# Performance work log

Measured on AMD Instinct MI355X. Metric: run time of the kernel, lower is better.

## Reference

```python
import jax, jax.numpy as jnp
import numpy as np

B, K, N, D, H, DD, NB, SEQ = 1, 512, 16384, 512, 64, 64, 10, 2048
COREF_PROP = 1  # config['coref_prop']
BIG = 1e23      # additive mask penalty from the torch code


def bucket_distance(d):
    # Lee et al. style log buckets: 0,1,2,3,4, [5-7], [8-15], [16-31], [32-63], [64+]
    d = jnp.abs(d)
    logb = jnp.floor(jnp.log2(jnp.maximum(d, 1).astype(jnp.float32))).astype(d.dtype) + 3
    return jnp.clip(jnp.where(d < 5, d, logb), 0, NB - 1)


def setup_inputs() -> dict:
    key = jax.random.key(0)
    ks = jax.random.split(key, 20)
    rng = np.random.default_rng(0)
    s = 0.02
    span_begin = jnp.sort(jax.random.randint(ks[2], (B, K), 0, SEQ), axis=-1)
    return dict(
        all_span_vecs=jax.random.normal(ks[0], (B, N, D), jnp.float32),
        span_vecs=jax.random.normal(ks[1], (B, K, D), jnp.float32),
        span_begin=span_begin,
        span_end=span_begin + jax.random.randint(ks[3], (B, K), 1, 10),
        triangular_mask=jnp.broadcast_to(jnp.tril(jnp.ones((K, K), jnp.float32), -1), (B, K, K)),
        span_scores=jax.random.normal(ks[4], (B, K, 1), jnp.float32),
        prune_indices=jnp.asarray(np.sort(np.stack([rng.choice(N, K, replace=False) for _ in range(B)]), axis=-1), jnp.int32),
        span_lengths=jnp.full((B,), K, jnp.int32),
        sequence_lengths=jnp.full((B,), SEQ, jnp.int32),
        Wl=jax.random.normal(ks[5], (D, H)) * s, bl=jnp.zeros((H,), jnp.float32),
        Wr=jax.random.normal(ks[6], (D, H)) * s, br=jnp.zeros((H,), jnp.float32),
        Wp=jax.random.normal(ks[7], (D, H)) * s,
        dist_emb=jax.random.normal(ks[8], (NB, DD)) * s,
        Wd=jax.random.normal(ks[9], (DD, H)) * s, bd=jnp.zeros((H,), jnp.float32),
        Wo=jax.random.normal(ks[10], (H, 1)) * s, bo=jnp.zeros((1,), jnp.float32),
        Wg1=jax.random.normal(ks[11], (2 * D, D)) * s, bg1=jnp.zeros((D,), jnp.float32),
        Wg2=jax.random.normal(ks[12], (2 * D, D)) * s, bg2=jnp.zeros((D,), jnp.float32),
        Wpr=jax.random.normal(ks[13], (D, 1)) * s, bpr=jnp.zeros((1,), jnp.float32),
    )


def reference(all_span_vecs, span_vecs, span_begin, span_end, triangular_mask,
              span_scores, prune_indices, span_lengths, sequence_lengths,
              Wl, bl, Wr, br, Wp, dist_emb, Wd, bd, Wo, bo,
              Wg1, bg1, Wg2, bg2, Wpr, bpr):
    # ----- OptFFpairs pairwise scorer: relu(left_i + right_j + prod(v_i*v_j) + dist_ij) -> scalar
    dist_idx = bucket_distance(span_begin[:, :, None] - span_begin[:, None, :])  # [B,K,K]
    dist_feat = dist_emb[dist_idx] @ Wd + bd                                     # [B,K,K,H]

    def pair_scores(u):
        left = u @ Wl + bl                                  # [B,K,H]
        right = u @ Wr + br                                 # [B,K,H]
        prod = jnp.einsum('bid,bjd,dh->bijh', u, u, Wp)     # avoids [B,K,K,D] intermediate
        h = jax.nn.relu(left[:, :, None, :] + right[:, None, :, :] + prod + dist_feat)
        return (h @ Wo + bo)[..., 0]                        # [B,K,K], i.e. squeeze(-1)

    eye = jnp.eye(K, dtype=span_vecs.dtype)[None]

    def add_scores(cs, ss):  # coref_add_scores: add span scores as rows+cols, zero diagonal
        cs = cs + ss + jnp.swapaxes(ss, -1, -2)
        return cs * (1.0 - eye)

    def gate(Wg, bg, left, right):  # MyGate: g = sigmoid(W[l;r]); g*l + (1-g)*r
        g = jax.nn.sigmoid(jnp.concatenate([left, right], -1) @ Wg + bg)
        return g * left + (1.0 - g) * right

    update = span_vecs
    cs = add_scores(pair_scores(update), span_scores)
    m1 = (1.0 - triangular_mask) * BIG
    m2 = (1.0 - jnp.swapaxes(triangular_mask, 1, 2)) * BIG
    for _ in range(COREF_PROP):
        p1 = jax.nn.softmax(cs - m1, axis=-1)
        p2 = jax.nn.softmax(cs - m2, axis=-1)
        c1 = p1 @ update
        c2 = p2 @ update
        update = gate(Wg1, bg1, update, c1) + gate(Wg2, bg2, update, c2)
        # update_coref_scores=True: rescore with pruner(update)
        cs = add_scores(pair_scores(update), update @ Wpr + bpr)

    # ----- overwrite_spans: masked scatter of updated filtered spans into all spans
    mask = (jnp.arange(K)[None, :] < span_lengths[:, None])[..., None]  # [B,K,1]
    b_idx = jnp.arange(B)[:, None]
    orig = all_span_vecs[b_idx, prune_indices]                          # [B,K,D]
    all_out = all_span_vecs.at[b_idx, prune_indices].set(jnp.where(mask, update, orig))
    return all_out, update, cs
```

## Files before the change

### kernel.cpp

```cpp
#include <hip/hip_runtime.h>
#include <hip/hip_bf16.h>


typedef __bf16 bf16;
typedef bf16 bf16x8 __attribute__((ext_vector_type(8)));
typedef float f32x4 __attribute__((ext_vector_type(4)));
typedef float f32x16 __attribute__((ext_vector_type(16)));

#define MFMA16(a, b, c) __builtin_amdgcn_mfma_f32_16x16x32_bf16((a), (b), (c), 0, 0, 0)
#define MFMA32(a, b, c) __builtin_amdgcn_mfma_f32_32x32x16_bf16((a), (b), (c), 0, 0, 0)

__device__ __forceinline__ void gll16(const bf16* g, bf16* lds) {
  __builtin_amdgcn_global_load_lds(
      (const __attribute__((address_space(1))) unsigned int*)g,
      (__attribute__((address_space(3))) unsigned int*)lds, 16, 0, 0);
}

__global__ void k_prep(const float* __restrict__ sv,
                       const float* __restrict__ Wl, const float* __restrict__ Wr,
                       const float* __restrict__ Wg1, const float* __restrict__ Wg2,
                       const float* __restrict__ de, const float* __restrict__ Wd,
                       const float* __restrict__ bd, const float* __restrict__ bl,
                       const float* __restrict__ br, const float* __restrict__ bg1,
                       const float* __restrict__ bg2, const float* __restrict__ Wp,
                       bf16* __restrict__ u1, bf16* __restrict__ ugb,
                       bf16* __restrict__ wlr, float* __restrict__ blbr,
                       float* __restrict__ bgc, bf16* __restrict__ wgb,
                       float* __restrict__ dtab, bf16* __restrict__ wpTb)
{
  const int total = 262144 + 65536 + 128 + 1048576 + 1024 + 640 + 32768;
  for (int idx0 = blockIdx.x * 256 + threadIdx.x; idx0 < total; idx0 += 2048 * 256) {
    int k = idx0;
    if (k < 262144) {
      float v = sv[k]; bf16 b = (bf16)v; u1[k] = b;
      int i = k >> 9, d = k & 511;
      ugb[(long)i * 1024 + d] = b;
      ugb[524288 + (long)i * 1024 + d] = b;
      continue;
    }
    k -= 262144;
    if (k < 65536) {
      int d = k >> 7, h = k & 127;
      wlr[k] = (bf16)(h < 64 ? Wl[d * 64 + h] : Wr[d * 64 + h - 64]);
      continue;
    }
    k -= 65536;
    if (k < 128) { blbr[k] = (k < 64 ? bl[k] : br[k - 64]); continue; }
    k -= 128;
    if (k < 1048576) {
      wgb[k] = (bf16)(k < 524288 ? Wg1[k] : Wg2[k - 524288]);
      continue;
    }
    k -= 1048576;
    if (k < 1024) { bgc[k] = (k < 512 ? bg1[k] : bg2[k - 512]); continue; }
    k -= 1024;
    if (k < 640) {
      int b_ = k >> 6, h = k & 63;
      float s = bd[h];
      for (int e = 0; e < 64; ++e) s += de[b_ * 64 + e] * Wd[e * 64 + h];
      dtab[k] = s;
      continue;
    }
    k -= 640;
    {
      int h = k >> 9, d = k & 511;
      wpTb[k] = (bf16)Wp[d * 64 + h];
    }
  }
}

__global__ __launch_bounds__(256, 2) void k_gemm(
    const bf16* __restrict__ A, int lda, long asz,
    const bf16* __restrict__ B, int ldb, long bsz,
    float* __restrict__ C, int ldc, long csz,
    const float* __restrict__ bias, int bstride, int K,
    bf16* __restrict__ xout)
{
  __shared__ bf16 As[64 * 40];
  __shared__ bf16 Bs[64 * 40];
  const int t = threadIdx.x, lane = t & 63, wave = t >> 6;
  const int tc = blockIdx.x, tr = blockIdx.y, z = blockIdx.z;
  A += (long)z * asz; B += (long)z * bsz; C += (long)z * csz;
  const int wr = wave >> 1, wc = wave & 1;
  const int arow = t >> 2, aslot = t & 3;
  const int s = lane >> 4, rr = lane & 15;
  f32x4 acc00 = {}, acc01 = {}, acc10 = {}, acc11 = {};
  const int nk = K >> 5;
  for (int kk = 0; kk < nk; ++kk) {
    __syncthreads();
    *(uint4*)&As[arow * 40 + aslot * 8] =
        *(const uint4*)(A + (long)(tr * 64 + arow) * lda + kk * 32 + aslot * 8);
    {
      const bf16* bsrc = B + (long)(kk * 32 + aslot * 8) * ldb + tc * 64 + arow;
      bf16x8 tv;
#pragma unroll
      for (int e = 0; e < 8; ++e) tv[e] = bsrc[(long)e * ldb];
      *(bf16x8*)&Bs[arow * 40 + aslot * 8] = tv;
    }
    __syncthreads();
    bf16x8 a0 = *(const bf16x8*)&As[(wr * 32 + rr) * 40 + s * 8];
    bf16x8 a1 = *(const bf16x8*)&As[(wr * 32 + 16 + rr) * 40 + s * 8];
    bf16x8 b0 = *(const bf16x8*)&Bs[(wc * 32 + rr) * 40 + s * 8];
    bf16x8 b1 = *(const bf16x8*)&Bs[(wc * 32 + 16 + rr) * 40 + s * 8];
    acc00 = MFMA16(a0, b0, acc00);
    acc01 = MFMA16(a0, b1, acc01);
    acc10 = MFMA16(a1, b0, acc10);
    acc11 = MFMA16(a1, b1, acc11);
  }
#pragma unroll
  for (int mf = 0; mf < 2; ++mf) {
#pragma unroll
    for (int nf = 0; nf < 2; ++nf) {
      f32x4 v = mf == 0 ? (nf == 0 ? acc00 : acc01) : (nf == 0 ? acc10 : acc11);
      int col = tc * 64 + wc * 32 + nf * 16 + rr;
      float bi = bias ? bias[z * bstride + col] : 0.f;
      int row0 = tr * 64 + wr * 32 + mf * 16 + s * 4;
#pragma unroll
      for (int r = 0; r < 4; ++r) {
        float val = v[r] + bi;
        int row = row0 + r;
        C[(long)row * ldc + col] = val;
        if (xout) {
          long gidx = (row < 512)
              ? ((long)row * 1024 + 512 + col)
              : (524288 + (long)(row - 512) * 1024 + 512 + col);
          xout[gidx] = (bf16)val;
        }
      }
    }
  }
}

__global__ __launch_bounds__(512, 2) void k_pair(
    const bf16* __restrict__ Ubf, const float* __restrict__ Uf,
    const bf16* __restrict__ wpTb, const float* __restrict__ LR,
    const float* __restrict__ dtabg, const int* __restrict__ sb,
    const float* __restrict__ ss, const float* __restrict__ Wo,
    const float* __restrict__ bo, float* __restrict__ cs,
    const float* __restrict__ copysrc, float* __restrict__ copydst, int docopy)
{
  __shared__ bf16 Apan[2][256 * 32];
  __shared__ bf16 Bpan[2][256 * 32];
  __shared__ float dtsp[10 * 68];
  __shared__ int sbt[256];

  const int t = threadIdx.x;
  const int l = t & 63;
  const int w = t >> 6;
  const int wm = w >> 1, wn = w & 1;
  const int hi = l >> 5, l31 = l & 31;
  const int jb = blockIdx.x;
  const int mt = blockIdx.y;
  const int i0 = mt * 4;
  const int i = i0 + wm;

  for (int idx = t; idx < 640; idx += 512)
    dtsp[(idx >> 6) * 68 + (idx & 63)] = dtabg[idx];
  if (t < 256) sbt[t] = sb[jb * 256 + t];

  const bf16 *bsrc0, *bsrc1;
  {
    int r0 = t >> 2, c0 = t & 3;
    int r1 = 128 + (t >> 2);
    bsrc0 = Ubf + (long)(jb * 256 + r0) * 512 + ((c0 ^ ((r0 >> 1) & 3)) * 8);
    bsrc1 = Ubf + (long)(jb * 256 + r1) * 512 + ((c0 ^ ((r1 >> 1) & 3)) * 8);
  }
  const int ar0 = t >> 2, ar1 = 128 + (t >> 2), as0 = t & 3;
  const int awb0 = ar0 * 64 + ((as0 ^ ((ar0 >> 1) & 3)) * 16);
  const int awb1 = ar1 * 64 + ((as0 ^ ((ar1 >> 1) & 3)) * 16);
  const float* ua0p = Uf + (long)(i0 + (ar0 >> 6)) * 512 + as0 * 8;
  const float* ua1p = Uf + (long)(i0 + (ar1 >> 6)) * 512 + as0 * 8;
  const bf16* wp0p = wpTb + (long)(ar0 & 63) * 512 + as0 * 8;
  const bf16* wp1p = wpTb + (long)(ar1 & 63) * 512 + as0 * 8;

  int aoff[2][2], boff[4][2];
#pragma unroll
  for (int rf = 0; rf < 2; ++rf)
#pragma unroll
    for (int ks = 0; ks < 2; ++ks) {
      int r = wm * 64 + rf * 32 + l31;
      aoff[rf][ks] = r * 64 + (((ks * 2 + hi) ^ ((r >> 1) & 3)) * 16);
    }
#pragma unroll
  for (int cf = 0; cf < 4; ++cf)
#pragma unroll
    for (int ks = 0; ks < 2; ++ks) {
      int r = wn * 128 + cf * 32 + l31;
      boff[cf][ks] = r * 64 + (((ks * 2 + hi) ^ ((r >> 1) & 3)) * 16);
    }

  {
    gll16(bsrc0, &Bpan[0][0 * 4096 + w * 512]);
    gll16(bsrc1, &Bpan[0][1 * 4096 + w * 512]);
    float4 a00 = *(const float4*)ua0p, a01 = *(const float4*)(ua0p + 4);
    float4 a10 = *(const float4*)ua1p, a11 = *(const float4*)(ua1p + 4);
    bf16x8 w0 = *(const bf16x8*)wp0p, w1 = *(const bf16x8*)wp1p;
    bf16x8 v0, v1;
#pragma unroll
    for (int e = 0; e < 4; ++e) {
      v0[e] = (bf16)(a00[e] * (float)w0[e]);
      v0[e + 4] = (bf16)(a01[e] * (float)w0[e + 4]);
      v1[e] = (bf16)(a10[e] * (float)w1[e]);
      v1[e + 4] = (bf16)(a11[e] * (float)w1[e + 4]);
    }
    *(bf16x8*)((char*)&Apan[0][0] + awb0) = v0;
    *(bf16x8*)((char*)&Apan[0][0] + awb1) = v1;
  }
  asm volatile("s_waitcnt vmcnt(0)");
  __syncthreads();

  f32x16 acc[2][4] = {};

  for (int kc = 0; kc < 16; ++kc) {
    const int cur = kc & 1;
    float4 nA00, nA01, nA10, nA11;
    bf16x8 nW0, nW1;
    if (kc < 15) {
      gll16(bsrc0 + (kc + 1) * 32, &Bpan[cur ^ 1][0 * 4096 + w * 512]);
      gll16(bsrc1 + (kc + 1) * 32, &Bpan[cur ^ 1][1 * 4096 + w * 512]);
      nA00 = *(const float4*)(ua0p + (kc + 1) * 32);
      nA01 = *(const float4*)(ua0p + (kc + 1) * 32 + 4);
      nA10 = *(const float4*)(ua1p + (kc + 1) * 32);
      nA11 = *(const float4*)(ua1p + (kc + 1) * 32 + 4);
      nW0 = *(const bf16x8*)(wp0p + (kc + 1) * 32);
      nW1 = *(const bf16x8*)(wp1p + (kc + 1) * 32);
    }
    const char* Ab = (const char*)&Apan[cur][0];
    const char* Bb = (const char*)&Bpan[cur][0];
#pragma unroll
    for (int ks = 0; ks < 2; ++ks) {
      bf16x8 af0 = *(const bf16x8*)(Ab + aoff[0][ks]);
      bf16x8 af1 = *(const bf16x8*)(Ab + aoff[1][ks]);
      bf16x8 bf0 = *(const bf16x8*)(Bb + boff[0][ks]);
      bf16x8 bf1 = *(const bf16x8*)(Bb + boff[1][ks]);
      bf16x8 bf2 = *(const bf16x8*)(Bb + boff[2][ks]);
      bf16x8 bf3 = *(const bf16x8*)(Bb + boff[3][ks]);
      __builtin_amdgcn_s_setprio(1);
      acc[0][0] = MFMA32(af0, bf0, acc[0][0]);
      acc[0][1] = MFMA32(af0, bf1, acc[0][1]);
      acc[0][2] = MFMA32(af0, bf2, acc[0][2]);
      acc[0][3] = MFMA32(af0, bf3, acc[0][3]);
      acc[1][0] = MFMA32(af1, bf0, acc[1][0]);
      acc[1][1] = MFMA32(af1, bf1, acc[1][1]);
      acc[1][2] = MFMA32(af1, bf2, acc[1][2]);
      acc[1][3] = MFMA32(af1, bf3, acc[1][3]);
      __builtin_amdgcn_s_setprio(0);
    }
    if (kc < 15) {
      asm volatile("s_waitcnt vmcnt(0)");
      bf16x8 v0, v1;
#pragma unroll
      for (int e = 0; e < 4; ++e) {
        v0[e] = (bf16)(nA00[e] * (float)nW0[e]);
        v0[e + 4] = (bf16)(nA01[e] * (float)nW0[e + 4]);
        v1[e] = (bf16)(nA10[e] * (float)nW1[e]);
        v1[e + 4] = (bf16)(nA11[e] * (float)nW1[e + 4]);
      }
      *(bf16x8*)((char*)&Apan[cur ^ 1][0] + awb0) = v0;
      *(bf16x8*)((char*)&Apan[cur ^ 1][0] + awb1) = v1;
    }
    __syncthreads();
  }

  float4 wo_t[2][4], lf_t[2][4];
#pragma unroll
  for (int rf = 0; rf < 2; ++rf)
#pragma unroll
    for (int g = 0; g < 4; ++g) {
      wo_t[rf][g] = *(const float4*)&Wo[rf * 32 + 4 * hi + 8 * g];
      lf_t[rf][g] = *(const float4*)&LR[i * 128 + rf * 32 + 4 * hi + 8 * g];
    }
  const float ssi = ss[i];
  const int sbi = sb[i];
  const float bo0 = bo[0];
#pragma unroll
  for (int cf = 0; cf < 4; ++cf) {
    int jl = wn * 128 + cf * 32 + l31;
    int j = jb * 256 + jl;
    int dd = sbi - sbt[jl];
    int ad = dd < 0 ? -dd : dd;
    int bkt = ad < 5 ? ad : (31 - __clz(ad)) + 3;
    bkt = bkt > 9 ? 9 : bkt;
    float ssj = ss[j];
    float sum = 0.f;
#pragma unroll
    for (int rf = 0; rf < 2; ++rf) {
#pragma unroll
      for (int g = 0; g < 4; ++g) {
        float4 dt4 = *(const float4*)&dtsp[bkt * 68 + rf * 32 + 4 * hi + 8 * g];
        float4 rt4 = *(const float4*)&LR[j * 128 + 64 + rf * 32 + 4 * hi + 8 * g];
#pragma unroll
        for (int e = 0; e < 4; ++e) {
          float v = acc[rf][cf][g * 4 + e] + lf_t[rf][g][e] + rt4[e] + dt4[e];
          v = fmaxf(v, 0.f);
          sum += v * wo_t[rf][g][e];
        }
      }
    }
    sum += __shfl_xor(sum, 32);
    float val = (j == i) ? 0.f : (sum + bo0 + ssi + ssj);
    if (hi == 0) cs[(long)i * 512 + j] = val;
  }

  if (docopy) {
    const float4* s4 = (const float4*)copysrc;
    float4* d4 = (float4*)copydst;
    int idx = (mt * 2 + jb) * 512 + t;
#pragma unroll
    for (int q = 0; q < 16; ++q)
      d4[(long)q * 131072 + idx] = s4[(long)q * 131072 + idx];
  }
}

__global__ __launch_bounds__(64) void k_softmax(const float* __restrict__ cs,
                                                bf16* __restrict__ p12)
{
  int b = blockIdx.x, kind = b >> 9, i = b & 511, lane = threadIdx.x;
  const float* row = cs + i * 512;
  float v[8];
  float4 x0 = *(const float4*)(row + lane * 8);
  float4 x1 = *(const float4*)(row + lane * 8 + 4);
  v[0] = x0.x; v[1] = x0.y; v[2] = x0.z; v[3] = x0.w;
  v[4] = x1.x; v[5] = x1.y; v[6] = x1.z; v[7] = x1.w;
  bool any = (kind == 0) ? (i > 0) : (i < 511);
  bf16x8 ov;
  if (!any) {
    float u = 1.0f / 512.0f;
#pragma unroll
    for (int e = 0; e < 8; ++e) ov[e] = (bf16)u;
  } else {
    float m = -3.4e38f;
#pragma unroll
    for (int e = 0; e < 8; ++e) {
      int jj = lane * 8 + e;
      bool valid = (kind == 0) ? (jj < i) : (jj > i);
      if (valid) m = fmaxf(m, v[e]);
    }
    m = fmaxf(m, __shfl_xor(m, 1));  m = fmaxf(m, __shfl_xor(m, 2));
    m = fmaxf(m, __shfl_xor(m, 4));  m = fmaxf(m, __shfl_xor(m, 8));
    m = fmaxf(m, __shfl_xor(m, 16)); m = fmaxf(m, __shfl_xor(m, 32));
    float p[8]; float ssum = 0.f;
#pragma unroll
    for (int e = 0; e < 8; ++e) {
      int jj = lane * 8 + e;
      bool valid = (kind == 0) ? (jj < i) : (jj > i);
      p[e] = valid ? __expf(v[e] - m) : 0.f;
      ssum += p[e];
    }
    ssum += __shfl_xor(ssum, 1);  ssum += __shfl_xor(ssum, 2);
    ssum += __shfl_xor(ssum, 4);  ssum += __shfl_xor(ssum, 8);
    ssum += __shfl_xor(ssum, 16); ssum += __shfl_xor(ssum, 32);
    float inv = 1.0f / ssum;
#pragma unroll
    for (int e = 0; e < 8; ++e) ov[e] = (bf16)(p[e] * inv);
  }
  *(bf16x8*)(p12 + (long)b * 512 + lane * 8) = ov;
}

__global__ __launch_bounds__(512) void k_mid2(
    const float* __restrict__ sv, const float* __restrict__ c12,
    const float* __restrict__ G12, const float* __restrict__ Wpr,
    const float* __restrict__ bpr, const bf16* __restrict__ wlr,
    const float* __restrict__ blbr, const int* __restrict__ pi,
    const int* __restrict__ sl, float* __restrict__ upd,
    bf16* __restrict__ u2, float* __restrict__ ss2,
    float* __restrict__ lr2, float* __restrict__ out_all)
{
  __shared__ float upl[512];
  __shared__ float red[8];
  __shared__ float part2[4][128];
  const int i = blockIdx.x;
  const int t = threadIdx.x;
  const long ii = (long)i * 512 + t;

  float u = sv[ii], c1 = c12[ii], c2 = c12[262144 + ii];
  float g1 = 1.f / (1.f + __expf(-G12[ii]));
  float g2 = 1.f / (1.f + __expf(-G12[262144 + ii]));
  float up = g1 * u + (1.f - g1) * c1 + g2 * u + (1.f - g2) * c2;
  upd[ii] = up;
  u2[ii] = (bf16)up;
  upl[t] = up;
  if (i < sl[0]) out_all[(long)pi[i] * 512 + t] = up;

  float pd = up * Wpr[t];
  pd += __shfl_xor(pd, 1);  pd += __shfl_xor(pd, 2);  pd += __shfl_xor(pd, 4);
  pd += __shfl_xor(pd, 8);  pd += __shfl_xor(pd, 16); pd += __shfl_xor(pd, 32);
  if ((t & 63) == 0) red[t >> 6] = pd;
  __syncthreads();
  if (t == 0) {
    float s = 0.f;
#pragma unroll
    for (int e = 0; e < 8; ++e) s += red[e];
    ss2[i] = s + bpr[0];
  }

  const int n = t & 127, part = t >> 7;
  float s = 0.f;
  const int d0 = part * 128;
#pragma unroll 4
  for (int d2 = 0; d2 < 128; ++d2)
    s += upl[d0 + d2] * (float)wlr[(d0 + d2) * 128 + n];
  part2[part][n] = s;
  __syncthreads();
  if (t < 128)
    lr2[(long)i * 128 + t] =
        part2[0][t] + part2[1][t] + part2[2][t] + part2[3][t] + blbr[t];
}

extern "C" void kernel_launch(void* const* d_in, const int* in_sizes, int n_in,
                              void* d_out, int out_size, void* d_ws, size_t ws_size,
                              hipStream_t stream)
{
  const float* asv = (const float*)d_in[0];
  const float* sv = (const float*)d_in[1];
  const int* sb = (const int*)d_in[2];
  const float* sscore = (const float*)d_in[5];
  const int* pi = (const int*)d_in[6];
  const int* sl = (const int*)d_in[7];
  const float* Wl = (const float*)d_in[9];
  const float* bl = (const float*)d_in[10];
  const float* Wr = (const float*)d_in[11];
  const float* br = (const float*)d_in[12];
  const float* Wp = (const float*)d_in[13];
  const float* de = (const float*)d_in[14];
  const float* Wd = (const float*)d_in[15];
  const float* bd = (const float*)d_in[16];
  const float* Wo = (const float*)d_in[17];
  const float* bo = (const float*)d_in[18];
  const float* Wg1 = (const float*)d_in[19];
  const float* bg1 = (const float*)d_in[20];
  const float* Wg2 = (const float*)d_in[21];
  const float* bg2 = (const float*)d_in[22];
  const float* Wpr = (const float*)d_in[23];
  const float* bpr = (const float*)d_in[24];

  float* out_all = (float*)d_out;
  float* out_upd = out_all + 8388608;
  float* out_cs = out_all + 8650752;

  char* w = (char*)d_ws;
  size_t off = 0;
  auto take = [&](size_t bytes) -> void* {
    void* p = w + off;
    off = (off + bytes + 255) & ~(size_t)255;
    return p;
  };
  bf16* u1b = (bf16*)take(524288);
  bf16* u2b = (bf16*)take(524288);
  bf16* wlr = (bf16*)take(131072);
  bf16* wgb = (bf16*)take(2097152);
  float* blbr = (float*)take(512);
  float* bgc = (float*)take(4096);
  float* dtab = (float*)take(2560);
  bf16* wpTb = (bf16*)take(65536);
  float* lr1 = (float*)take(262144);
  float* lr2 = (float*)take(262144);
  float* cs1 = (float*)take(1048576);
  bf16* p12 = (bf16*)take(1048576);
  float* c12 = (float*)take(4194304);
  bf16* ugb = (bf16*)take(2097152);
  float* G12 = (float*)take(2097152);
  float* ss2 = (float*)take(2048);

  k_prep<<<2048, 256, 0, stream>>>(sv, Wl, Wr, Wg1, Wg2, de, Wd, bd, bl, br, bg1, bg2,
                                   Wp, u1b, ugb, wlr, blbr, bgc, wgb, dtab, wpTb);
  k_gemm<<<dim3(2, 8, 1), 256, 0, stream>>>(u1b, 512, 0, wlr, 128, 0, lr1, 128, 0,
                                            blbr, 0, 512, nullptr);
  k_pair<<<dim3(2, 128), 512, 0, stream>>>(u1b, sv, wpTb, lr1, dtab, sb, sscore, Wo,
                                           bo, cs1, asv, out_all, 1);
  k_softmax<<<1024, 64, 0, stream>>>(cs1, p12);
  k_gemm<<<dim3(8, 16, 1), 256, 0, stream>>>(p12, 512, 0, u1b, 512, 0, c12, 512, 0,
                                             nullptr, 0, 512, ugb);
  k_gemm<<<dim3(8, 8, 2), 256, 0, stream>>>(ugb, 1024, 524288, wgb, 512, 524288,
                                            G12, 512, 262144, bgc, 512, 1024, nullptr);
  k_mid2<<<512, 512, 0, stream>>>(sv, c12, G12, Wpr, bpr, wlr, blbr, pi, sl,
                                  out_upd, u2b, ss2, lr2, out_all);
  k_pair<<<dim3(2, 128), 512, 0, stream>>>(u2b, out_upd, wpTb, lr2, dtab, sb, ss2, Wo,
                                           bo, out_cs, nullptr, nullptr, 0);
}
```

Measured before the change: 148.1 us.

## Add triple-buffered pair-scoring kernel for second rescoring pass

Adds k_pair2, a variant of the pairwise scoring kernel used for the second scoring pass. It keeps three LDS buffers, loads B panels asynchronously into LDS two steps ahead, and builds the A operand (u_i * Wp product, converted to bf16) in registers one step ahead, so the MFMA loop overlaps with global loads. It also drops the copy path that only the first call needs. The cost is more LDS use, hand-placed waitcnt values, and a launch bound that allows one block per CU.

New measurement: 146.0 us. About the same (-1.4%).

```diff
diff --git a/kernel.cpp b/kernel.cpp
--- a/kernel.cpp
+++ b/kernel.cpp
@@ -309,6 +309,185 @@
 #pragma unroll
     for (int q = 0; q < 16; ++q)
       d4[(long)q * 131072 + idx] = s4[(long)q * 131072 + idx];
+  }
+}
+
+#define P2_BUILD(DST, A00, A01, A10, A11, W0, W1)                \
+  {                                                              \
+    bf16x8 v0, v1;                                               \
+    _Pragma("unroll") for (int e = 0; e < 4; ++e) {              \
+      v0[e] = (bf16)((A00)[e] * (float)(W0)[e]);                 \
+      v0[e + 4] = (bf16)((A01)[e] * (float)(W0)[e + 4]);         \
+      v1[e] = (bf16)((A10)[e] * (float)(W1)[e]);                 \
+      v1[e + 4] = (bf16)((A11)[e] * (float)(W1)[e + 4]);         \
+    }                                                            \
+    *(bf16x8*)((DST) + awb0) = v0;                               \
+    *(bf16x8*)((DST) + awb1) = v1;                               \
+  }
+
+#define P2_ITER(KC, bA00, bA01, bA10, bA11, bW0, bW1, rA00, rA01, rA10, rA11, rW0, rW1) \
+  {                                                                                     \
+    const int bcur = (KC) % 3, bnxt = ((KC) + 1) % 3, bpre = ((KC) + 2) % 3;            \
+    asm volatile("s_waitcnt lgkmcnt(0)");                                               \
+    asm volatile("s_waitcnt vmcnt(14)");                                                \
+    __builtin_amdgcn_sched_barrier(0);                                                  \
+    __builtin_amdgcn_s_barrier();                                                       \
+    const char* Ab = Abase + bcur * 16384;                                              \
+    const char* Bb = Bbase + bcur * 16384;                                              \
+    _Pragma("unroll") for (int ks = 0; ks < 2; ++ks) {                                  \
+      bf16x8 af0 = *(const bf16x8*)(Ab + aoff[0][ks]);                                  \
+      bf16x8 af1 = *(const bf16x8*)(Ab + aoff[1][ks]);                                  \
+      bf16x8 bf0 = *(const bf16x8*)(Bb + boff[0][ks]);                                  \
+      bf16x8 bf1 = *(const bf16x8*)(Bb + boff[1][ks]);                                  \
+      bf16x8 bf2 = *(const bf16x8*)(Bb + boff[2][ks]);                                  \
+      bf16x8 bf3 = *(const bf16x8*)(Bb + boff[3][ks]);                                  \
+      __builtin_amdgcn_s_setprio(1);                                                    \
+      acc[0][0] = MFMA32(af0, bf0, acc[0][0]);                                          \
+      acc[0][1] = MFMA32(af0, bf1, acc[0][1]);                                          \
+      acc[0][2] = MFMA32(af0, bf2, acc[0][2]);                                          \
+      acc[0][3] = MFMA32(af0, bf3, acc[0][3]);                                          \
+      acc[1][0] = MFMA32(af1, bf0, acc[1][0]);                                          \
+      acc[1][1] = MFMA32(af1, bf1, acc[1][1]);                                          \
+      acc[1][2] = MFMA32(af1, bf2, acc[1][2]);                                          \
+      acc[1][3] = MFMA32(af1, bf3, acc[1][3]);                                          \
+      __builtin_amdgcn_s_setprio(0);                                                    \
+    }                                                                                   \
+    if ((KC) < 15) { P2_BUILD(Abase + bnxt * 16384, bA00, bA01, bA10, bA11, bW0, bW1) } \
+    if ((KC) < 14) {                                                                    \
+      bf16* Bd = (bf16*)(Bbase + bpre * 16384);                                         \
+      gll16(bsrc0 + ((KC) + 2) * 32, Bd + w * 512);                                     \
+      gll16(bsrc1 + ((KC) + 2) * 32, Bd + 4096 + w * 512);                              \
+      rA00 = *(const float4*)(ua0p + ((KC) + 2) * 32);                                  \
+      rA01 = *(const float4*)(ua0p + ((KC) + 2) * 32 + 4);                              \
+      rA10 = *(const float4*)(ua1p + ((KC) + 2) * 32);                                  \
+      rA11 = *(const float4*)(ua1p + ((KC) + 2) * 32 + 4);                              \
+      rW0 = *(const bf16x8*)(wp0p + ((KC) + 2) * 32);                                   \
+      rW1 = *(const bf16x8*)(wp1p + ((KC) + 2) * 32);                                   \
+    }                                                                                   \
+  }
+
+__global__ __launch_bounds__(512, 1) void k_pair2(
+    const bf16* __restrict__ Ubf, const float* __restrict__ Uf,
+    const bf16* __restrict__ wpTb, const float* __restrict__ LR,
+    const float* __restrict__ dtabg, const int* __restrict__ sb,
+    const float* __restrict__ ss, const float* __restrict__ Wo,
+    const float* __restrict__ bo, float* __restrict__ cs)
+{
+  __shared__ bf16 Apan[3][256 * 32];
+  __shared__ bf16 Bpan[3][256 * 32];
+  __shared__ float dtsp[10 * 68];
+  __shared__ int sbt[256];
+
+  const int t = threadIdx.x;
+  const int l = t & 63;
+  const int w = t >> 6;
+  const int wm = w >> 1, wn = w & 1;
+  const int hi = l >> 5, l31 = l & 31;
+  const int jb = blockIdx.x;
+  const int mt = blockIdx.y;
+  const int i0 = mt * 4;
+  const int i = i0 + wm;
+
+  for (int idx = t; idx < 640; idx += 512)
+    dtsp[(idx >> 6) * 68 + (idx & 63)] = dtabg[idx];
+  if (t < 256) sbt[t] = sb[jb * 256 + t];
+
+  const bf16 *bsrc0, *bsrc1;
+  {
+    int r0 = t >> 2, c0 = t & 3;
+    int r1 = 128 + (t >> 2);
+    bsrc0 = Ubf + (long)(jb * 256 + r0) * 512 + ((c0 ^ ((r0 >> 1) & 3)) * 8);
+    bsrc1 = Ubf + (long)(jb * 256 + r1) * 512 + ((c0 ^ ((r1 >> 1) & 3)) * 8);
+  }
+  const int ar0 = t >> 2, ar1 = 128 + (t >> 2), as0 = t & 3;
+  const int awb0 = ar0 * 64 + ((as0 ^ ((ar0 >> 1) & 3)) * 16);
+  const int awb1 = ar1 * 64 + ((as0 ^ ((ar1 >> 1) & 3)) * 16);
+  const float* ua0p = Uf + (long)(i0 + (ar0 >> 6)) * 512 + as0 * 8;
+  const float* ua1p = Uf + (long)(i0 + (ar1 >> 6)) * 512 + as0 * 8;
+  const bf16* wp0p = wpTb + (long)(ar0 & 63) * 512 + as0 * 8;
+  const bf16* wp1p = wpTb + (long)(ar1 & 63) * 512 + as0 * 8;
+
+  int aoff[2][2], boff[4][2];
+#pragma unroll
+  for (int rf = 0; rf < 2; ++rf)
+#pragma unroll
+    for (int ks = 0; ks < 2; ++ks) {
+      int r = wm * 64 + rf * 32 + l31;
+      aoff[rf][ks] = r * 64 + (((ks * 2 + hi) ^ ((r >> 1) & 3)) * 16);
+    }
+#pragma unroll
+  for (int cf = 0; cf < 4; ++cf)
+#pragma unroll
+    for (int ks = 0; ks < 2; ++ks) {
+      int r = wn * 128 + cf * 32 + l31;
+      boff[cf][ks] = r * 64 + (((ks * 2 + hi) ^ ((r >> 1) & 3)) * 16);
+    }
+
+  char* Abase = (char*)&Apan[0][0];
+  char* Bbase = (char*)&Bpan[0][0];
+
+  float4 aA00, aA01, aA10, aA11; bf16x8 wA0, wA1;
+  float4 aB00, aB01, aB10, aB11; bf16x8 wB0, wB1;
+  gll16(bsrc0, (bf16*)Bbase + w * 512);
+  gll16(bsrc1, (bf16*)Bbase + 4096 + w * 512);
+  aA00 = *(const float4*)ua0p;        aA01 = *(const float4*)(ua0p + 4);
+  aA10 = *(const float4*)ua1p;        aA11 = *(const float4*)(ua1p + 4);
+  wA0 = *(const bf16x8*)wp0p;         wA1 = *(const bf16x8*)wp1p;
+  gll16(bsrc0 + 32, (bf16*)(Bbase + 16384) + w * 512);
+  gll16(bsrc1 + 32, (bf16*)(Bbase + 16384) + 4096 + w * 512);
+  aB00 = *(const float4*)(ua0p + 32); aB01 = *(const float4*)(ua0p + 36);
+  aB10 = *(const float4*)(ua1p + 32); aB11 = *(const float4*)(ua1p + 36);
+  wB0 = *(const bf16x8*)(wp0p + 32);  wB1 = *(const bf16x8*)(wp1p + 32);
+  P2_BUILD(Abase, aA00, aA01, aA10, aA11, wA0, wA1)
+
+  f32x16 acc[2][4] = {};
+
+  for (int kq = 0; kq < 8; ++kq) {
+    const int kc = kq * 2;
+    P2_ITER(kc, aB00, aB01, aB10, aB11, wB0, wB1,
+            aA00, aA01, aA10, aA11, wA0, wA1)
+    P2_ITER(kc + 1, aA00, aA01, aA10, aA11, wA0, wA1,
+            aB00, aB01, aB10, aB11, wB0, wB1)
+  }
+
+  float4 wo_t[2][4], lf_t[2][4];
+#pragma unroll
+  for (int rf = 0; rf < 2; ++rf)
+#pragma unroll
+    for (int g = 0; g < 4; ++g) {
+      wo_t[rf][g] = *(const float4*)&Wo[rf * 32 + 4 * hi + 8 * g];
+      lf_t[rf][g] = *(const float4*)&LR[i * 128 + rf * 32 + 4 * hi + 8 * g];
+    }
+  const float ssi = ss[i];
+  const int sbi = sb[i];
+  const float bo0 = bo[0];
+#pragma unroll
+  for (int cf = 0; cf < 4; ++cf) {
+    int jl = wn * 128 + cf * 32 + l31;
+    int j = jb * 256 + jl;
+    int dd = sbi - sbt[jl];
+    int ad = dd < 0 ? -dd : dd;
+    int bkt = ad < 5 ? ad : (31 - __clz(ad)) + 3;
+    bkt = bkt > 9 ? 9 : bkt;
+    float ssj = ss[j];
+    float sum = 0.f;
+#pragma unroll
+    for (int rf = 0; rf < 2; ++rf) {
+#pragma unroll
+      for (int g = 0; g < 4; ++g) {
+        float4 dt4 = *(const float4*)&dtsp[bkt * 68 + rf * 32 + 4 * hi + 8 * g];
+        float4 rt4 = *(const float4*)&LR[j * 128 + 64 + rf * 32 + 4 * hi + 8 * g];
+#pragma unroll
+        for (int e = 0; e < 4; ++e) {
+          float v = acc[rf][cf][g * 4 + e] + lf_t[rf][g][e] + rt4[e] + dt4[e];
+          v = fmaxf(v, 0.f);
+          sum += v * wo_t[rf][g][e];
+        }
+      }
+    }
+    sum += __shfl_xor(sum, 32);
+    float val = (j == i) ? 0.f : (sum + bo0 + ssi + ssj);
+    if (hi == 0) cs[(long)i * 512 + j] = val;
   }
 }
 
@@ -475,6 +654,6 @@
                                             G12, 512, 262144, bgc, 512, 1024, nullptr);
   k_mid2<<<512, 512, 0, stream>>>(sv, c12, G12, Wpr, bpr, wlr, blbr, pi, sl,
                                   out_upd, u2b, ss2, lr2, out_all);
-  k_pair<<<dim3(2, 128), 512, 0, stream>>>(u2b, out_upd, wpTb, lr2, dtab, sb, ss2, Wo,
-                                           bo, out_cs, nullptr, nullptr, 0);
-}
+  k_pair2<<<dim3(2, 128), 512, 0, stream>>>(u2b, out_upd, wpTb, lr2, dtab, sb, ss2,
+                                            Wo, bo, out_cs);
+}
```
